# Optimization experiments

Hardware: AMD Instinct MI355X
Metric: run time of the kernel (lower is better)

Reference implementation:

```python
import jax, jax.numpy as jnp
import numpy as np
from jax import lax

NT, TL = 32, 64           # num_trajs, traj_length
H, W, C = 84, 84, 4       # Atari frame stack
SIZE = 256                # LSTM hidden size
NOUT = 18                 # num_outputs
FEAT = 6 * 6 * 32         # after four stride-2 SAME convs: 84->42->21->11->6
DN = ('NHWC', 'HWIO', 'NHWC')


def setup_inputs() -> dict:
    key = jax.random.key(0)
    ks = jax.random.split(key, 8)
    d = {}
    d['inputs'] = jax.random.normal(ks[0], (NT * TL, H, W, C), jnp.float32)
    cin = C
    for i in range(4):
        d[f'w{i+1}'] = jax.random.normal(ks[1 + i], (3, 3, cin, 32), jnp.float32) * 0.1
        d[f'b{i+1}'] = jnp.zeros((32,), jnp.float32)
        cin = 32
    d['lstm_w'] = jax.random.normal(ks[5], (FEAT + SIZE, 4 * SIZE), jnp.float32) * 0.05
    d['lstm_b'] = jnp.zeros((4 * SIZE,), jnp.float32)
    d['fc_w'] = jax.random.normal(ks[6], (SIZE, NOUT), jnp.float32) * 0.01
    d['fc_b'] = jnp.zeros((NOUT,), jnp.float32)
    d['c0'] = jnp.zeros((NT, SIZE), jnp.float32)
    d['h0'] = jnp.zeros((NT, SIZE), jnp.float32)
    return d


def reference(inputs, w1, b1, w2, b2, w3, b3, w4, b4,
              lstm_w, lstm_b, fc_w, fc_b, c0, h0):
    x = inputs
    for w, b in ((w1, b1), (w2, b2), (w3, b3), (w4, b4)):
        x = jax.nn.elu(lax.conv_general_dilated(
            x, w, window_strides=(2, 2), padding='SAME',
            dimension_numbers=DN) + b)
    # [NT*TL, 6, 6, 32] -> [TL, NT, FEAT] (time-major for scan)
    xs = x.reshape(NT, TL, FEAT).transpose(1, 0, 2)

    def step(carry, xt):
        c, h = carry
        gates = jnp.concatenate([xt, h], axis=-1) @ lstm_w + lstm_b
        i, j, f, o = jnp.split(gates, 4, axis=-1)
        # BasicLSTMCell with forget_bias = 1.0
        new_c = c * jax.nn.sigmoid(f + 1.0) + jax.nn.sigmoid(i) * jnp.tanh(j)
        new_h = jnp.tanh(new_c) * jax.nn.sigmoid(o)
        return (new_c, new_h), new_h

    _, outs = lax.scan(step, (c0, h0), xs)          # outs: [TL, NT, SIZE]
    feats = outs.transpose(1, 0, 2).reshape(-1, SIZE)  # batch-major flatten
    logits = feats @ fc_w + fc_b                    # [NT*TL, NOUT]
    return logits
```

## Files before the change

### kernel.cpp

```cpp
#include <hip/hip_runtime.h>
#include <math.h>

#define NTRAJ 32
#define TLEN  64
#define BATCH (NTRAJ*TLEN)

__device__ __forceinline__ float eluf(float x){ return x > 0.f ? x : expm1f(x); }
__device__ __forceinline__ float sigmf(float x){ return 1.f/(1.f+expf(-x)); }

__global__ __launch_bounds__(256) void conv1_kernel(
    const float* __restrict__ in,
    const float* __restrict__ w,
    const float* __restrict__ b,
    float* __restrict__ out)
{
    int pos = blockIdx.x*256 + threadIdx.x;
    int n   = pos / (42*42);
    int rem = pos % (42*42);
    int oy  = rem / 42, ox = rem % 42;
    float acc[32];
    #pragma unroll
    for(int o=0;o<32;o++) acc[o] = b[o];
    for(int ky=0; ky<3; ky++){
        int iy = 2*oy + ky;
        if(iy >= 84) continue;
        for(int kx=0; kx<3; kx++){
            int ix = 2*ox + kx;
            if(ix >= 84) continue;
            float4 v = *(const float4*)(in + (((n*84 + iy)*84) + ix)*4);
            const float* wq = w + (ky*3 + kx)*128;
            #pragma unroll
            for(int o=0;o<32;o++) acc[o] += v.x*wq[o];
            #pragma unroll
            for(int o=0;o<32;o++) acc[o] += v.y*wq[32+o];
            #pragma unroll
            for(int o=0;o<32;o++) acc[o] += v.z*wq[64+o];
            #pragma unroll
            for(int o=0;o<32;o++) acc[o] += v.w*wq[96+o];
        }
    }
    const int NPOS = BATCH*42*42;
    #pragma unroll
    for(int o=0;o<32;o++) out[o*NPOS + pos] = eluf(acc[o]);
}

template<int IH, int IW, int OH, int OW, int PB>
__global__ __launch_bounds__(256) void convN_kernel(
    const float* __restrict__ in,
    const float* __restrict__ w,
    const float* __restrict__ b,
    float* __restrict__ out)
{
    const int IPLANE = BATCH*IH*IW;
    const int OPLANE = BATCH*OH*OW;
    int pos = blockIdx.x*256 + threadIdx.x;
    if(pos >= OPLANE) return;
    int n   = pos / (OH*OW);
    int rem = pos % (OH*OW);
    int oy  = rem / OW, ox = rem % OW;
    float acc[32];
    #pragma unroll
    for(int o=0;o<32;o++) acc[o] = b[o];
    for(int ky=0; ky<3; ky++){
        int iy = 2*oy + ky - PB;
        if(iy < 0 || iy >= IH) continue;
        for(int kx=0; kx<3; kx++){
            int ix = 2*ox + kx - PB;
            if(ix < 0 || ix >= IW) continue;
            const float* ip = in + (n*IH + iy)*IW + ix;
            const float* wp = w + (ky*3 + kx)*1024;
            for(int ci=0; ci<32; ci+=4){
                float x0 = ip[(ci+0)*IPLANE];
                float x1 = ip[(ci+1)*IPLANE];
                float x2 = ip[(ci+2)*IPLANE];
                float x3 = ip[(ci+3)*IPLANE];
                const float* wq = wp + ci*32;
                #pragma unroll
                for(int o=0;o<32;o++) acc[o] += x0*wq[o];
                #pragma unroll
                for(int o=0;o<32;o++) acc[o] += x1*wq[32+o];
                #pragma unroll
                for(int o=0;o<32;o++) acc[o] += x2*wq[64+o];
                #pragma unroll
                for(int o=0;o<32;o++) acc[o] += x3*wq[96+o];
            }
        }
    }
    #pragma unroll
    for(int o=0;o<32;o++) out[o*OPLANE + pos] = eluf(acc[o]);
}

__global__ __launch_bounds__(256) void relayout_kernel(
    const float* __restrict__ p4,
    float* __restrict__ at)
{
    int i = blockIdx.x*256 + threadIdx.x;
    int f = i >> 11, r = i & 2047;
    int s = f >> 5,  c = f & 31;
    int t = r >> 5,  n = r & 31;
    int nt = n*64 + t;
    at[i] = p4[c*(BATCH*36) + nt*36 + s];
}

__global__ __launch_bounds__(256) void gx_gemm_kernel(
    const float* __restrict__ at,
    const float* __restrict__ lw,
    const float* __restrict__ lb,
    float* __restrict__ gx,
    unsigned int* __restrict__ bar)
{
    if(blockIdx.x == 0 && blockIdx.y == 0 && threadIdx.x == 0) *bar = 0u;
    int lane = threadIdx.x & 63;
    int wv   = threadIdx.x >> 6;
    int r0   = blockIdx.x * 16;
    int oc   = blockIdx.y*256 + wv*64 + lane;
    float acc[16];
    float bias = lb[oc];
    #pragma unroll
    for(int i=0;i<16;i++) acc[i] = bias;
    #pragma unroll 4
    for(int k=0;k<1152;k++){
        float wval = lw[k*1024 + oc];
        const float* ap = at + k*2048 + r0;
        #pragma unroll
        for(int i=0;i<16;i++) acc[i] += ap[i] * wval;
    }
    #pragma unroll
    for(int i=0;i<16;i++) gx[(r0+i)*1024 + oc] = acc[i];
}

__global__ __launch_bounds__(256) void lstm_coop_kernel(
    const float* __restrict__ gx,
    const float* __restrict__ lw,
    const float* __restrict__ c0,
    const float* __restrict__ h0,
    float* __restrict__ feats,
    float* __restrict__ hbuf,
    unsigned int* __restrict__ bar)
{
    __shared__ float hs[32*256];
    __shared__ float wl2[32*256];
    float* const gl = hs;

    const int wg = blockIdx.x;
    const int t  = threadIdx.x;
    const int c    = t & 31;
    const int ngrp = t >> 3 >> 2;
    const int gcol = (c>>3)*256 + wg*8 + (c&7);
    const float* wh = lw + 1152*1024;

    #pragma unroll
    for(int i=0;i<32;i++){
        int e = t + 256*i;
        int k = e >> 5, cc = e & 31;
        int gc = (cc>>3)*256 + wg*8 + (cc&7);
        wl2[(k>>1)*64 + cc*2 + (k&1)] = wh[k*1024 + gc];
    }
    const int un = t >> 3, uu = t & 7;
    float cst = c0[un*256 + wg*8 + uu];

    const float2* wv  = (const float2*)wl2;
    float4* hs4 = (float4*)hs;

    for(int st=0; st<64; ++st){
        const float4* hp4 = (const float4*)((st == 0) ? h0 : (hbuf + ((st&1)^1)*8192));
        #pragma unroll
        for(int i=0;i<8;i++){
            int q = t + 256*i;
            hs4[q] = hp4[q];
        }
        int rbase = st*32 + ngrp*4;
        float gx0 = gx[(rbase+0)*1024 + gcol];
        float gx1 = gx[(rbase+1)*1024 + gcol];
        float gx2 = gx[(rbase+2)*1024 + gcol];
        float gx3 = gx[(rbase+3)*1024 + gcol];
        __syncthreads();
        float a0 = 0.f, a1 = 0.f, a2 = 0.f, a3 = 0.f;
        const float4* h0r = hs4 + (ngrp*4+0)*64;
        const float4* h1r = hs4 + (ngrp*4+1)*64;
        const float4* h2r = hs4 + (ngrp*4+2)*64;
        const float4* h3r = hs4 + (ngrp*4+3)*64;
        #pragma unroll 4
        for(int k4=0;k4<64;k4++){
            float2 wa = wv[(2*k4+0)*32 + c];
            float2 wb = wv[(2*k4+1)*32 + c];
            float4 hv0 = h0r[k4], hv1 = h1r[k4], hv2 = h2r[k4], hv3 = h3r[k4];
            a0 += hv0.x*wa.x + hv0.y*wa.y + hv0.z*wb.x + hv0.w*wb.y;
            a1 += hv1.x*wa.x + hv1.y*wa.y + hv1.z*wb.x + hv1.w*wb.y;
            a2 += hv2.x*wa.x + hv2.y*wa.y + hv2.z*wb.x + hv2.w*wb.y;
            a3 += hv3.x*wa.x + hv3.y*wa.y + hv3.z*wb.x + hv3.w*wb.y;
        }
        __syncthreads();
        gl[(ngrp*4+0)*33 + c] = a0 + gx0;
        gl[(ngrp*4+1)*33 + c] = a1 + gx1;
        gl[(ngrp*4+2)*33 + c] = a2 + gx2;
        gl[(ngrp*4+3)*33 + c] = a3 + gx3;
        __syncthreads();
        {
            float i_ = gl[un*33 +      uu];
            float j_ = gl[un*33 +  8 + uu];
            float f_ = gl[un*33 + 16 + uu];
            float o_ = gl[un*33 + 24 + uu];
            cst = cst*sigmf(f_ + 1.f) + sigmf(i_)*tanhf(j_);
            float h = tanhf(cst)*sigmf(o_);
            int col = wg*8 + uu;
            hbuf[(st&1)*8192 + un*256 + col] = h;
            feats[(un*64 + st)*256 + col]    = h;
        }
        if(st != 63){
            __syncthreads();
            if(t == 0){
                unsigned tgt = (unsigned)(st+1)*32u;
                __hip_atomic_fetch_add(bar, 1u, __ATOMIC_ACQ_REL, __HIP_MEMORY_SCOPE_AGENT);
                unsigned spins = 0;
                while(__hip_atomic_load(bar, __ATOMIC_ACQUIRE, __HIP_MEMORY_SCOPE_AGENT) < tgt){
                    __builtin_amdgcn_s_sleep(2);
                    if(++spins > 20000000u) break;
                }
            }
            __syncthreads();
        }
    }
}

__global__ __launch_bounds__(64) void fc_kernel(
    const float* __restrict__ feats, const float* __restrict__ fw,
    const float* __restrict__ fb,    float* __restrict__ out)
{
    __shared__ float h[256];
    int p = blockIdx.x, t = threadIdx.x;
    *(float4*)&h[t*4] = *(const float4*)(feats + p*256 + t*4);
    __syncthreads();
    if(t < 18){
        float acc = fb[t];
        for(int k=0;k<256;k++) acc += h[k]*fw[k*18 + t];
        out[p*18 + t] = acc;
    }
}

extern "C" void kernel_launch(void* const* d_in, const int* in_sizes, int n_in,
                              void* d_out, int out_size, void* d_ws, size_t ws_size,
                              hipStream_t stream) {
    const float* inp = (const float*)d_in[0];
    const float* w1  = (const float*)d_in[1];  const float* b1 = (const float*)d_in[2];
    const float* w2  = (const float*)d_in[3];  const float* b2 = (const float*)d_in[4];
    const float* w3  = (const float*)d_in[5];  const float* b3 = (const float*)d_in[6];
    const float* w4  = (const float*)d_in[7];  const float* b4 = (const float*)d_in[8];
    const float* lw  = (const float*)d_in[9];  const float* lb = (const float*)d_in[10];
    const float* fw  = (const float*)d_in[11]; const float* fb = (const float*)d_in[12];
    const float* c0  = (const float*)d_in[13]; const float* h0 = (const float*)d_in[14];
    float* out = (float*)d_out;
    float* ws  = (float*)d_ws;

    const size_t n1 = (size_t)32*3612672;
    const size_t n3 = (size_t)32*247808;
    const size_t n4 = (size_t)32*73728;

    float* p1 = ws;
    float* p2 = p1 + n1;
    float* p3 = ws;
    float* p4 = p3 + n3;
    float* at = p4 + n4;
    float* gxb   = at  + (size_t)1152*2048;
    float* feats = gxb + (size_t)2048*1024;
    float* hbuf  = feats + (size_t)2048*256;
    unsigned int* bar = (unsigned int*)(hbuf + 2*32*256);

    conv1_kernel<<<14112,256,0,stream>>>(inp, w1, b1, p1);
    convN_kernel<42,42,21,21,0><<<3528,256,0,stream>>>(p1, w2, b2, p2);
    convN_kernel<21,21,11,11,1><<<968,256,0,stream>>>(p2, w3, b3, p3);
    convN_kernel<11,11, 6, 6,1><<<288,256,0,stream>>>(p3, w4, b4, p4);
    relayout_kernel<<<9216,256,0,stream>>>(p4, at);
    gx_gemm_kernel<<<dim3(128,4),256,0,stream>>>(at, lw, lb, gxb, bar);
    lstm_coop_kernel<<<32,256,0,stream>>>(gxb, lw, c0, h0, feats, hbuf, bar);
    fc_kernel<<<2048,64,0,stream>>>(feats, fw, fb, out);
}
```

Baseline: 1.930 ms.

## Switch conv activations to NHWC, swizzle block order, use per-block flag barrier

```diff
diff --git a/kernel.cpp b/kernel.cpp
--- a/kernel.cpp
+++ b/kernel.cpp
@@ -14,7 +14,9 @@
     const float* __restrict__ b,
     float* __restrict__ out)
 {
-    int pos = blockIdx.x*256 + threadIdx.x;
+    int bid = blockIdx.x;
+    bid = (bid & 7)*1764 + (bid >> 3);
+    int pos = bid*256 + threadIdx.x;
     int n   = pos / (42*42);
     int rem = pos % (42*42);
     int oy  = rem / 42, ox = rem % 42;
@@ -39,9 +41,11 @@
             for(int o=0;o<32;o++) acc[o] += v.w*wq[96+o];
         }
     }
-    const int NPOS = BATCH*42*42;
-    #pragma unroll
-    for(int o=0;o<32;o++) out[o*NPOS + pos] = eluf(acc[o]);
+    float4* op = (float4*)(out + (size_t)pos*32);
+    #pragma unroll
+    for(int q=0;q<8;q++)
+        op[q] = make_float4(eluf(acc[4*q]), eluf(acc[4*q+1]),
+                            eluf(acc[4*q+2]), eluf(acc[4*q+3]));
 }
 
 template<int IH, int IW, int OH, int OW, int PB>
@@ -51,10 +55,11 @@
     const float* __restrict__ b,
     float* __restrict__ out)
 {
-    const int IPLANE = BATCH*IH*IW;
-    const int OPLANE = BATCH*OH*OW;
-    int pos = blockIdx.x*256 + threadIdx.x;
-    if(pos >= OPLANE) return;
+    int bid = blockIdx.x;
+    const int cpx = gridDim.x >> 3;
+    bid = (bid & 7)*cpx + (bid >> 3);
+    int pos = bid*256 + threadIdx.x;
+    if(pos >= BATCH*OH*OW) return;
     int n   = pos / (OH*OW);
     int rem = pos % (OH*OW);
     int oy  = rem / OW, ox = rem % OW;
@@ -67,27 +72,28 @@
         for(int kx=0; kx<3; kx++){
             int ix = 2*ox + kx - PB;
             if(ix < 0 || ix >= IW) continue;
-            const float* ip = in + (n*IH + iy)*IW + ix;
+            const float4* ip = (const float4*)(in + ((size_t)(n*IH + iy)*IW + ix)*32);
             const float* wp = w + (ky*3 + kx)*1024;
-            for(int ci=0; ci<32; ci+=4){
-                float x0 = ip[(ci+0)*IPLANE];
-                float x1 = ip[(ci+1)*IPLANE];
-                float x2 = ip[(ci+2)*IPLANE];
-                float x3 = ip[(ci+3)*IPLANE];
-                const float* wq = wp + ci*32;
-                #pragma unroll
-                for(int o=0;o<32;o++) acc[o] += x0*wq[o];
-                #pragma unroll
-                for(int o=0;o<32;o++) acc[o] += x1*wq[32+o];
-                #pragma unroll
-                for(int o=0;o<32;o++) acc[o] += x2*wq[64+o];
-                #pragma unroll
-                for(int o=0;o<32;o++) acc[o] += x3*wq[96+o];
+            #pragma unroll
+            for(int c4=0;c4<8;c4++){
+                float4 x = ip[c4];
+                const float* wq = wp + c4*128;
+                #pragma unroll
+                for(int o=0;o<32;o++) acc[o] += x.x*wq[o];
+                #pragma unroll
+                for(int o=0;o<32;o++) acc[o] += x.y*wq[32+o];
+                #pragma unroll
+                for(int o=0;o<32;o++) acc[o] += x.z*wq[64+o];
+                #pragma unroll
+                for(int o=0;o<32;o++) acc[o] += x.w*wq[96+o];
             }
         }
     }
-    #pragma unroll
-    for(int o=0;o<32;o++) out[o*OPLANE + pos] = eluf(acc[o]);
+    float4* op = (float4*)(out + (size_t)pos*32);
+    #pragma unroll
+    for(int q=0;q<8;q++)
+        op[q] = make_float4(eluf(acc[4*q]), eluf(acc[4*q+1]),
+                            eluf(acc[4*q+2]), eluf(acc[4*q+3]));
 }
 
 __global__ __launch_bounds__(256) void relayout_kernel(
@@ -96,10 +102,9 @@
 {
     int i = blockIdx.x*256 + threadIdx.x;
     int f = i >> 11, r = i & 2047;
-    int s = f >> 5,  c = f & 31;
-    int t = r >> 5,  n = r & 31;
-    int nt = n*64 + t;
-    at[i] = p4[c*(BATCH*36) + nt*36 + s];
+    int tt = r >> 5, n = r & 31;
+    int nt = n*64 + tt;
+    at[i] = p4[nt*1152 + f];
 }
 
 __global__ __launch_bounds__(256) void gx_gemm_kernel(
@@ -109,7 +114,8 @@
     float* __restrict__ gx,
     unsigned int* __restrict__ bar)
 {
-    if(blockIdx.x == 0 && blockIdx.y == 0 && threadIdx.x == 0) *bar = 0u;
+    if(blockIdx.x == 0 && blockIdx.y == 0 && threadIdx.x < 32)
+        bar[threadIdx.x*32] = 0u;
     int lane = threadIdx.x & 63;
     int wv   = threadIdx.x >> 6;
     int r0   = blockIdx.x * 16;
@@ -145,7 +151,7 @@
     const int wg = blockIdx.x;
     const int t  = threadIdx.x;
     const int c    = t & 31;
-    const int ngrp = t >> 3 >> 2;
+    const int ngrp = t >> 5;
     const int gcol = (c>>3)*256 + wg*8 + (c&7);
     const float* wh = lw + 1152*1024;
 
@@ -209,12 +215,15 @@
         }
         if(st != 63){
             __syncthreads();
-            if(t == 0){
-                unsigned tgt = (unsigned)(st+1)*32u;
-                __hip_atomic_fetch_add(bar, 1u, __ATOMIC_ACQ_REL, __HIP_MEMORY_SCOPE_AGENT);
+            if(t == 0)
+                __hip_atomic_store(bar + wg*32, (unsigned)(st+1),
+                                   __ATOMIC_RELEASE, __HIP_MEMORY_SCOPE_AGENT);
+            if(t < 32){
+                unsigned tgt = (unsigned)(st+1);
                 unsigned spins = 0;
-                while(__hip_atomic_load(bar, __ATOMIC_ACQUIRE, __HIP_MEMORY_SCOPE_AGENT) < tgt){
-                    __builtin_amdgcn_s_sleep(2);
+                while(__hip_atomic_load(bar + t*32, __ATOMIC_ACQUIRE,
+                                        __HIP_MEMORY_SCOPE_AGENT) < tgt){
+                    __builtin_amdgcn_s_sleep(1);
                     if(++spins > 20000000u) break;
                 }
             }
```

Result: faster. 1.843 ms (-4.5%).
